# Optimization experiments

Hardware: AMD Instinct MI355X
Metric: run time of the kernel (lower is better)

The kernel has to match this reference:

```python
import jax, jax.numpy as jnp
import numpy as np

N = 100000  # num nodes


def gcn_conv(x, edge_index, W, b):
    # PyG GCNConv (eval): x' = D^-1/2 (A + I) D^-1/2 (x @ W) + b
    x = x @ W  # [N, out]
    row = jnp.concatenate([edge_index[0], jnp.arange(N)])  # sources (+ self loops)
    col = jnp.concatenate([edge_index[1], jnp.arange(N)])  # targets (+ self loops)
    ones = jnp.ones(row.shape[0], dtype=x.dtype)
    deg = jax.ops.segment_sum(ones, col, num_segments=N)
    dis = jnp.where(deg > 0, jax.lax.rsqrt(jnp.maximum(deg, 1.0)), 0.0)
    norm = dis[row] * dis[col]  # [E+N]
    msg = norm[:, None] * x[row]  # gather + scale
    out = jax.ops.segment_sum(msg, col, num_segments=N)  # scatter-add
    return out + b


def setup_inputs() -> dict:
    key = jax.random.key(0)
    k1, k2, k3, k4 = jax.random.split(key, 4)
    F_in, H, F_out = 512, 16, 40
    x = jax.random.normal(k1, (N, F_in), dtype=jnp.float32)
    edge_index = jax.random.randint(k2, (2, 3200000), 0, N, dtype=jnp.int64)
    W1 = jax.random.normal(k3, (F_in, H), dtype=jnp.float32) / np.sqrt(F_in)
    b1 = jnp.zeros((H,), dtype=jnp.float32)
    W2 = jax.random.normal(k4, (H, F_out), dtype=jnp.float32) / np.sqrt(H)
    b2 = jnp.zeros((F_out,), dtype=jnp.float32)
    return {"x": x, "edge_index": edge_index, "W1": W1, "b1": b1, "W2": W2, "b2": b2}


def reference(x, edge_index, W1, b1, W2, b2):
    # eval mode: no drop_edge, no dropout
    h = jax.nn.relu(gcn_conv(x, edge_index, W1, b1))
    return gcn_conv(h, edge_index, W2, b2)
```

## Files before the change

kernel.cpp:

```cpp
#include <hip/hip_runtime.h>

#define F_IN 512
#define HDIM 16
#define F_OUT 40

__device__ __forceinline__ int load_idx(const void* ei, int is64, long long i) {
  if (is64) return (int)((const long long*)ei)[i];
  return ((const int*)ei)[i];
}

extern "C" __global__ void k_init(int* __restrict__ cnt, int n, int* __restrict__ flag) {
  int i = blockIdx.x * blockDim.x + threadIdx.x;
  if (i < n) cnt[i] = 0;
  if (i == 0) *flag = 1;
}

extern "C" __global__ void k_detect(const unsigned int* __restrict__ w, int npairs,
                                    int* __restrict__ flag) {
  int i = blockIdx.x * blockDim.x + threadIdx.x;
  if (i < npairs && w[2 * i + 1] != 0u) atomicAnd(flag, 0);
}

extern "C" __global__ void k_deg(const void* __restrict__ ei, int E, int* __restrict__ cnt,
                                 const int* __restrict__ flag) {
  int e = blockIdx.x * blockDim.x + threadIdx.x;
  if (e >= E) return;
  int is64 = *flag;
  int c = load_idx(ei, is64, (long long)E + e);
  atomicAdd(&cnt[c], 1);
}

extern "C" __global__ void k_dis(const int* __restrict__ cnt, float* __restrict__ dis, int n) {
  int i = blockIdx.x * blockDim.x + threadIdx.x;
  if (i < n) dis[i] = rsqrtf((float)cnt[i] + 1.0f);
}

extern "C" __global__ void k_scan1(const int* __restrict__ cnt, int* __restrict__ offs,
                                   int* __restrict__ bsum, int n) {
  __shared__ int sh[256];
  int tid = threadIdx.x;
  int i = blockIdx.x * 256 + tid;
  int v = (i < n) ? cnt[i] : 0;
  sh[tid] = v;
  __syncthreads();
  for (int d = 1; d < 256; d <<= 1) {
    int t = (tid >= d) ? sh[tid - d] : 0;
    __syncthreads();
    sh[tid] += t;
    __syncthreads();
  }
  if (i < n) offs[i] = sh[tid] - v;
  if (tid == 255) bsum[blockIdx.x] = sh[255];
}

extern "C" __global__ void k_scan2(int* __restrict__ bsum, int nb) {
  __shared__ int sh[512];
  int tid = threadIdx.x;
  int v = (tid < nb) ? bsum[tid] : 0;
  sh[tid] = v;
  __syncthreads();
  for (int d = 1; d < 512; d <<= 1) {
    int t = (tid >= d) ? sh[tid - d] : 0;
    __syncthreads();
    sh[tid] += t;
    __syncthreads();
  }
  if (tid < nb) bsum[tid] = sh[tid] - v;
}

extern "C" __global__ void k_scan3(int* __restrict__ offs, int* __restrict__ cur,
                                   const int* __restrict__ bsum, int n) {
  int i = blockIdx.x * blockDim.x + threadIdx.x;
  if (i < n) {
    int o = offs[i] + bsum[i >> 8];
    offs[i] = o;
    cur[i] = o;
  }
}

extern "C" __global__ void k_scatter(const void* __restrict__ ei, int E, int* __restrict__ cur,
                                     int* __restrict__ srcbuf, const int* __restrict__ flag) {
  int e = blockIdx.x * blockDim.x + threadIdx.x;
  if (e >= E) return;
  int is64 = *flag;
  int r = load_idx(ei, is64, e);
  int c = load_idx(ei, is64, (long long)E + e);
  int p = atomicAdd(&cur[c], 1);
  srcbuf[p] = r;
}

extern "C" __global__ __launch_bounds__(256) void k_mm1(
    const float* __restrict__ x, const float* __restrict__ W1, float* __restrict__ h1, int n) {
  int r = blockIdx.x * 256 + threadIdx.x;
  if (r >= n) return;
  const float4* xr = (const float4*)(x + (long long)r * F_IN);
  float acc[HDIM];
#pragma unroll
  for (int j = 0; j < HDIM; j++) acc[j] = 0.f;
  for (int k4 = 0; k4 < F_IN / 4; k4++) {
    float4 xv = xr[k4];
    float xk[4] = {xv.x, xv.y, xv.z, xv.w};
#pragma unroll
    for (int kk = 0; kk < 4; kk++) {
      const float4* wr = (const float4*)(W1 + (long long)(4 * k4 + kk) * HDIM);
#pragma unroll
      for (int q = 0; q < HDIM / 4; q++) {
        float4 wv = wr[q];
        acc[4 * q + 0] = fmaf(xk[kk], wv.x, acc[4 * q + 0]);
        acc[4 * q + 1] = fmaf(xk[kk], wv.y, acc[4 * q + 1]);
        acc[4 * q + 2] = fmaf(xk[kk], wv.z, acc[4 * q + 2]);
        acc[4 * q + 3] = fmaf(xk[kk], wv.w, acc[4 * q + 3]);
      }
    }
  }
  float4* o = (float4*)(h1 + (long long)r * HDIM);
#pragma unroll
  for (int q = 0; q < HDIM / 4; q++)
    o[q] = make_float4(acc[4 * q], acc[4 * q + 1], acc[4 * q + 2], acc[4 * q + 3]);
}

extern "C" __global__ void k_agg(const float* __restrict__ hin, const int* __restrict__ offs,
                                 const int* __restrict__ cnt, const int* __restrict__ srcbuf,
                                 const float* __restrict__ dis, const float* __restrict__ bias,
                                 int do_relu, float* __restrict__ hout, int n) {
  int t = blockIdx.x * blockDim.x + threadIdx.x;
  int i = t >> 4, j = t & 15;
  if (i >= n) return;
  int beg = offs[i];
  int c = cnt[i];
  float di = dis[i];
  float acc = 0.f;
  for (int p = 0; p < c; p++) {
    int s = srcbuf[beg + p];
    acc = fmaf(dis[s], hin[(long long)s * HDIM + j], acc);
  }
  float v = di * acc + di * di * hin[(long long)i * HDIM + j];
  if (bias) v += bias[j];
  if (do_relu) v = fmaxf(v, 0.f);
  hout[(long long)i * HDIM + j] = v;
}

extern "C" __global__ __launch_bounds__(256) void k_mm2(
    const float* __restrict__ a2, const float* __restrict__ W2, const float* __restrict__ b2,
    float* __restrict__ out, int n) {
  int r = blockIdx.x * 256 + threadIdx.x;
  if (r >= n) return;
  float a[HDIM];
  const float4* ar = (const float4*)(a2 + (long long)r * HDIM);
#pragma unroll
  for (int q = 0; q < HDIM / 4; q++) {
    float4 v = ar[q];
    a[4 * q] = v.x; a[4 * q + 1] = v.y; a[4 * q + 2] = v.z; a[4 * q + 3] = v.w;
  }
  float acc[F_OUT];
#pragma unroll
  for (int j = 0; j < F_OUT; j++) acc[j] = b2[j];
#pragma unroll
  for (int k = 0; k < HDIM; k++) {
    float ak = a[k];
    const float4* wr = (const float4*)(W2 + k * F_OUT);
#pragma unroll
    for (int q = 0; q < F_OUT / 4; q++) {
      float4 wv = wr[q];
      acc[4 * q + 0] = fmaf(ak, wv.x, acc[4 * q + 0]);
      acc[4 * q + 1] = fmaf(ak, wv.y, acc[4 * q + 1]);
      acc[4 * q + 2] = fmaf(ak, wv.z, acc[4 * q + 2]);
      acc[4 * q + 3] = fmaf(ak, wv.w, acc[4 * q + 3]);
    }
  }
  float4* o = (float4*)(out + (long long)r * F_OUT);
#pragma unroll
  for (int q = 0; q < F_OUT / 4; q++)
    o[q] = make_float4(acc[4 * q], acc[4 * q + 1], acc[4 * q + 2], acc[4 * q + 3]);
}

extern "C" void kernel_launch(void* const* d_in, const int* in_sizes, int n_in,
                              void* d_out, int out_size, void* d_ws, size_t ws_size,
                              hipStream_t stream) {
  const float* x = (const float*)d_in[0];
  const void* ei = d_in[1];
  const float* W1 = (const float*)d_in[2];
  const float* b1 = (const float*)d_in[3];
  const float* W2 = (const float*)d_in[4];
  const float* b2 = (const float*)d_in[5];
  float* out = (float*)d_out;

  const int n = in_sizes[0] / F_IN;
  const int E = in_sizes[1] / 2;

  char* w = (char*)d_ws;
  auto alloc = [&](size_t bytes) {
    char* p = w;
    w += (bytes + 255) & ~(size_t)255;
    return p;
  };
  int* cnt = (int*)alloc((size_t)n * 4);
  int* offs = (int*)alloc((size_t)n * 4);
  int* cur = (int*)alloc((size_t)n * 4);
  float* dis = (float*)alloc((size_t)n * 4);
  int* flag = (int*)alloc(4);
  int* bsum = (int*)alloc(512 * 4);
  int* srcb = (int*)alloc((size_t)E * 4);
  float* h1 = (float*)alloc((size_t)n * HDIM * 4);
  float* z = (float*)alloc((size_t)n * HDIM * 4);
  float* a2 = (float*)alloc((size_t)n * HDIM * 4);

  int nb = (n + 255) / 256;
  dim3 B(256);
  hipLaunchKernelGGL(k_init, dim3(nb), B, 0, stream, cnt, n, flag);
  int npairs = 4096;
  if (npairs > E) npairs = E;
  hipLaunchKernelGGL(k_detect, dim3((npairs + 255) / 256), B, 0, stream,
                     (const unsigned int*)ei, npairs, flag);
  hipLaunchKernelGGL(k_deg, dim3((E + 255) / 256), B, 0, stream, ei, E, cnt, flag);
  hipLaunchKernelGGL(k_dis, dim3(nb), B, 0, stream, cnt, dis, n);
  hipLaunchKernelGGL(k_scan1, dim3(nb), B, 0, stream, cnt, offs, bsum, n);
  hipLaunchKernelGGL(k_scan2, dim3(1), dim3(512), 0, stream, bsum, nb);
  hipLaunchKernelGGL(k_scan3, dim3(nb), B, 0, stream, offs, cur, bsum, n);
  hipLaunchKernelGGL(k_scatter, dim3((E + 255) / 256), B, 0, stream, ei, E, cur, srcb, flag);
  hipLaunchKernelGGL(k_mm1, dim3(nb), B, 0, stream, x, W1, h1, n);
  hipLaunchKernelGGL(k_agg, dim3((n * 16 + 255) / 256), B, 0, stream, h1, offs, cnt, srcb, dis,
                     b1, 1, z, n);
  hipLaunchKernelGGL(k_agg, dim3((n * 16 + 255) / 256), B, 0, stream, z, offs, cnt, srcb, dis,
                     (const float*)nullptr, 0, a2, n);
  hipLaunchKernelGGL(k_mm2, dim3(nb), B, 0, stream, a2, W2, b2, out, n);
}
```

Baseline: 807.3 us.

## Replace per-node CSR with 64-target buckets and shared-memory atomic aggregation

Drops the exact per-node CSR sort, which needed a three-kernel scan and one contended atomic per edge on each node's cursor. Edges are now grouped into buckets of 64 target nodes, with 4 replicated counters per bucket to spread atomic contention, and each edge stores its source and local target packed into one 32-bit word. Aggregation runs one block per bucket and accumulates in shared memory with LDS atomics, removing the per-node serial loop and its load imbalance. The packing assumes source ids fit in 20 bits, and the bucket order makes float summation order non-deterministic.

```diff
diff --git a/kernel.cpp b/kernel.cpp
--- a/kernel.cpp
+++ b/kernel.cpp
@@ -3,15 +3,19 @@
 #define F_IN 512
 #define HDIM 16
 #define F_OUT 40
+#define BTGT 64
+#define REPL 4
 
 __device__ __forceinline__ int load_idx(const void* ei, int is64, long long i) {
   if (is64) return (int)((const long long*)ei)[i];
   return ((const int*)ei)[i];
 }
 
-extern "C" __global__ void k_init(int* __restrict__ cnt, int n, int* __restrict__ flag) {
+extern "C" __global__ void k_init(int* __restrict__ cnt, int n, int* __restrict__ hist, int m,
+                                  int* __restrict__ flag) {
   int i = blockIdx.x * blockDim.x + threadIdx.x;
   if (i < n) cnt[i] = 0;
+  if (i < m) hist[i] = 0;
   if (i == 0) *flag = 1;
 }
 
@@ -21,13 +25,15 @@
   if (i < npairs && w[2 * i + 1] != 0u) atomicAnd(flag, 0);
 }
 
-extern "C" __global__ void k_deg(const void* __restrict__ ei, int E, int* __restrict__ cnt,
-                                 const int* __restrict__ flag) {
+extern "C" __global__ void k_hist(const void* __restrict__ ei, int E, int* __restrict__ cnt,
+                                  int* __restrict__ hist, const int* __restrict__ flag) {
   int e = blockIdx.x * blockDim.x + threadIdx.x;
   if (e >= E) return;
   int is64 = *flag;
   int c = load_idx(ei, is64, (long long)E + e);
   atomicAdd(&cnt[c], 1);
+  int idx = (c >> 6) * REPL + (blockIdx.x & (REPL - 1));
+  atomicAdd(&hist[idx], 1);
 }
 
 extern "C" __global__ void k_dis(const int* __restrict__ cnt, float* __restrict__ dis, int n) {
@@ -35,58 +41,50 @@
   if (i < n) dis[i] = rsqrtf((float)cnt[i] + 1.0f);
 }
 
-extern "C" __global__ void k_scan1(const int* __restrict__ cnt, int* __restrict__ offs,
-                                   int* __restrict__ bsum, int n) {
-  __shared__ int sh[256];
+extern "C" __global__ __launch_bounds__(1024) void k_scanb(const int* __restrict__ hist,
+                                                           int* __restrict__ boffs,
+                                                           int* __restrict__ bcur, int M) {
+  __shared__ int sh[1024];
   int tid = threadIdx.x;
-  int i = blockIdx.x * 256 + tid;
-  int v = (i < n) ? cnt[i] : 0;
-  sh[tid] = v;
+  int C = (M + 1023) / 1024;
+  int base = tid * C;
+  int s = 0;
+  for (int k = 0; k < C; k++) {
+    int idx = base + k;
+    if (idx < M) s += hist[idx];
+  }
+  sh[tid] = s;
   __syncthreads();
-  for (int d = 1; d < 256; d <<= 1) {
+  for (int d = 1; d < 1024; d <<= 1) {
     int t = (tid >= d) ? sh[tid - d] : 0;
     __syncthreads();
     sh[tid] += t;
     __syncthreads();
   }
-  if (i < n) offs[i] = sh[tid] - v;
-  if (tid == 255) bsum[blockIdx.x] = sh[255];
-}
-
-extern "C" __global__ void k_scan2(int* __restrict__ bsum, int nb) {
-  __shared__ int sh[512];
-  int tid = threadIdx.x;
-  int v = (tid < nb) ? bsum[tid] : 0;
-  sh[tid] = v;
-  __syncthreads();
-  for (int d = 1; d < 512; d <<= 1) {
-    int t = (tid >= d) ? sh[tid - d] : 0;
-    __syncthreads();
-    sh[tid] += t;
-    __syncthreads();
-  }
-  if (tid < nb) bsum[tid] = sh[tid] - v;
-}
-
-extern "C" __global__ void k_scan3(int* __restrict__ offs, int* __restrict__ cur,
-                                   const int* __restrict__ bsum, int n) {
-  int i = blockIdx.x * blockDim.x + threadIdx.x;
-  if (i < n) {
-    int o = offs[i] + bsum[i >> 8];
-    offs[i] = o;
-    cur[i] = o;
-  }
-}
-
-extern "C" __global__ void k_scatter(const void* __restrict__ ei, int E, int* __restrict__ cur,
-                                     int* __restrict__ srcbuf, const int* __restrict__ flag) {
+  int run = sh[tid] - s;
+  for (int k = 0; k < C; k++) {
+    int idx = base + k;
+    if (idx < M) {
+      int v = hist[idx];
+      boffs[idx] = run;
+      bcur[idx] = run;
+      run += v;
+    }
+  }
+  if (tid == 1023) boffs[M] = run;
+}
+
+extern "C" __global__ void k_bucket(const void* __restrict__ ei, int E, int* __restrict__ bcur,
+                                    unsigned int* __restrict__ bked,
+                                    const int* __restrict__ flag) {
   int e = blockIdx.x * blockDim.x + threadIdx.x;
   if (e >= E) return;
   int is64 = *flag;
   int r = load_idx(ei, is64, e);
   int c = load_idx(ei, is64, (long long)E + e);
-  int p = atomicAdd(&cur[c], 1);
-  srcbuf[p] = r;
+  int idx = (c >> 6) * REPL + (blockIdx.x & (REPL - 1));
+  int p = atomicAdd(&bcur[idx], 1);
+  bked[p] = (unsigned int)r | ((unsigned int)(c & (BTGT - 1)) << 20);
 }
 
 extern "C" __global__ __launch_bounds__(256) void k_mm1(
@@ -119,25 +117,36 @@
     o[q] = make_float4(acc[4 * q], acc[4 * q + 1], acc[4 * q + 2], acc[4 * q + 3]);
 }
 
-extern "C" __global__ void k_agg(const float* __restrict__ hin, const int* __restrict__ offs,
-                                 const int* __restrict__ cnt, const int* __restrict__ srcbuf,
-                                 const float* __restrict__ dis, const float* __restrict__ bias,
-                                 int do_relu, float* __restrict__ hout, int n) {
-  int t = blockIdx.x * blockDim.x + threadIdx.x;
-  int i = t >> 4, j = t & 15;
-  if (i >= n) return;
-  int beg = offs[i];
-  int c = cnt[i];
-  float di = dis[i];
-  float acc = 0.f;
-  for (int p = 0; p < c; p++) {
-    int s = srcbuf[beg + p];
-    acc = fmaf(dis[s], hin[(long long)s * HDIM + j], acc);
-  }
-  float v = di * acc + di * di * hin[(long long)i * HDIM + j];
-  if (bias) v += bias[j];
-  if (do_relu) v = fmaxf(v, 0.f);
-  hout[(long long)i * HDIM + j] = v;
+extern "C" __global__ __launch_bounds__(256) void k_agg(
+    const float* __restrict__ hin, const unsigned int* __restrict__ bked,
+    const int* __restrict__ boffs, const float* __restrict__ dis,
+    const float* __restrict__ bias, int do_relu, float* __restrict__ hout, int n) {
+  __shared__ float acc[BTGT * HDIM];
+  int b = blockIdx.x;
+  int t = threadIdx.x;
+  int g = t >> 4;
+  int j = t & 15;
+  for (int k = t; k < BTGT * HDIM; k += 256) acc[k] = 0.f;
+  __syncthreads();
+  int beg = boffs[b * REPL];
+  int end = boffs[(b + 1) * REPL];
+  for (int p = beg + g; p < end; p += 16) {
+    unsigned int pk = bked[p];
+    int s = (int)(pk & 0xFFFFFu);
+    int lc = (int)(pk >> 20);
+    float v = dis[s] * hin[(long long)s * HDIM + j];
+    atomicAdd(&acc[lc * HDIM + j], v);
+  }
+  __syncthreads();
+  for (int il = g; il < BTGT; il += 16) {
+    int i = b * BTGT + il;
+    if (i >= n) break;
+    float di = dis[i];
+    float v = di * acc[il * HDIM + j] + di * di * hin[(long long)i * HDIM + j];
+    if (bias) v += bias[j];
+    if (do_relu) v = fmaxf(v, 0.f);
+    hout[(long long)i * HDIM + j] = v;
+  }
 }
 
 extern "C" __global__ __launch_bounds__(256) void k_mm2(
@@ -154,7 +163,7 @@
   }
   float acc[F_OUT];
 #pragma unroll
-  for (int j = 0; j < F_OUT; j++) acc[j] = b2[j];
+  for (int jj = 0; jj < F_OUT; jj++) acc[jj] = b2[jj];
 #pragma unroll
   for (int k = 0; k < HDIM; k++) {
     float ak = a[k];
@@ -187,6 +196,8 @@
 
   const int n = in_sizes[0] / F_IN;
   const int E = in_sizes[1] / 2;
+  const int NB = (n + BTGT - 1) / BTGT;
+  const int M = NB * REPL;
 
   char* w = (char*)d_ws;
   auto alloc = [&](size_t bytes) {
@@ -195,33 +206,30 @@
     return p;
   };
   int* cnt = (int*)alloc((size_t)n * 4);
-  int* offs = (int*)alloc((size_t)n * 4);
-  int* cur = (int*)alloc((size_t)n * 4);
   float* dis = (float*)alloc((size_t)n * 4);
   int* flag = (int*)alloc(4);
-  int* bsum = (int*)alloc(512 * 4);
-  int* srcb = (int*)alloc((size_t)E * 4);
+  int* hist = (int*)alloc((size_t)M * 4);
+  int* boffs = (int*)alloc((size_t)(M + 1) * 4);
+  int* bcur = (int*)alloc((size_t)M * 4);
+  unsigned int* bked = (unsigned int*)alloc((size_t)E * 4);
   float* h1 = (float*)alloc((size_t)n * HDIM * 4);
   float* z = (float*)alloc((size_t)n * HDIM * 4);
   float* a2 = (float*)alloc((size_t)n * HDIM * 4);
 
-  int nb = (n + 255) / 256;
   dim3 B(256);
-  hipLaunchKernelGGL(k_init, dim3(nb), B, 0, stream, cnt, n, flag);
+  int nbi = ((n > M ? n : M) + 255) / 256;
+  hipLaunchKernelGGL(k_init, dim3(nbi), B, 0, stream, cnt, n, hist, M, flag);
   int npairs = 4096;
   if (npairs > E) npairs = E;
   hipLaunchKernelGGL(k_detect, dim3((npairs + 255) / 256), B, 0, stream,
                      (const unsigned int*)ei, npairs, flag);
-  hipLaunchKernelGGL(k_deg, dim3((E + 255) / 256), B, 0, stream, ei, E, cnt, flag);
-  hipLaunchKernelGGL(k_dis, dim3(nb), B, 0, stream, cnt, dis, n);
-  hipLaunchKernelGGL(k_scan1, dim3(nb), B, 0, stream, cnt, offs, bsum, n);
-  hipLaunchKernelGGL(k_scan2, dim3(1), dim3(512), 0, stream, bsum, nb);
-  hipLaunchKernelGGL(k_scan3, dim3(nb), B, 0, stream, offs, cur, bsum, n);
-  hipLaunchKernelGGL(k_scatter, dim3((E + 255) / 256), B, 0, stream, ei, E, cur, srcb, flag);
-  hipLaunchKernelGGL(k_mm1, dim3(nb), B, 0, stream, x, W1, h1, n);
-  hipLaunchKernelGGL(k_agg, dim3((n * 16 + 255) / 256), B, 0, stream, h1, offs, cnt, srcb, dis,
-                     b1, 1, z, n);
-  hipLaunchKernelGGL(k_agg, dim3((n * 16 + 255) / 256), B, 0, stream, z, offs, cnt, srcb, dis,
+  hipLaunchKernelGGL(k_hist, dim3((E + 255) / 256), B, 0, stream, ei, E, cnt, hist, flag);
+  hipLaunchKernelGGL(k_dis, dim3((n + 255) / 256), B, 0, stream, cnt, dis, n);
+  hipLaunchKernelGGL(k_scanb, dim3(1), dim3(1024), 0, stream, hist, boffs, bcur, M);
+  hipLaunchKernelGGL(k_bucket, dim3((E + 255) / 256), B, 0, stream, ei, E, bcur, bked, flag);
+  hipLaunchKernelGGL(k_mm1, dim3((n + 255) / 256), B, 0, stream, x, W1, h1, n);
+  hipLaunchKernelGGL(k_agg, dim3(NB), B, 0, stream, h1, bked, boffs, dis, b1, 1, z, n);
+  hipLaunchKernelGGL(k_agg, dim3(NB), B, 0, stream, z, bked, boffs, dis,
                      (const float*)nullptr, 0, a2, n);
-  hipLaunchKernelGGL(k_mm2, dim3(nb), B, 0, stream, a2, W2, b2, out, n);
-}
+  hipLaunchKernelGGL(k_mm2, dim3((n + 255) / 256), B, 0, stream, a2, W2, b2, out, n);
+}
```

New measurement: 1.210 ms. 1.5x slower.
